# Kernel tuning notes

Hardware: AMD Instinct MI355X
Metric: run time of the kernel (lower is better)

## Reference

```python
import jax, jax.numpy as jnp
import numpy as np

B, T, U = 8, 200, 50
EPROJS = 512
DUNITS = 512
EMB = 512
JOINT = 512
ODIM = 1000
BLANK = 0


def setup_inputs() -> dict:
    key = jax.random.key(0)
    ks = jax.random.split(key, 16)
    s = lambda k, shape: (jax.random.normal(k, shape, jnp.float32) * 0.05)
    inp = {
        "hs_pad": jax.random.normal(ks[0], (B, T, EPROJS), jnp.float32),
        "ys_in_pad": jax.random.randint(ks[1], (B, U), 0, ODIM),
        "emb": s(ks[2], (ODIM, EMB)),
        "W_ih_0": s(ks[3], (4 * DUNITS, EMB)),
        "W_hh_0": s(ks[4], (4 * DUNITS, DUNITS)),
        "b_ih_0": s(ks[5], (4 * DUNITS,)),
        "b_hh_0": s(ks[6], (4 * DUNITS,)),
        "W_ih_1": s(ks[7], (4 * DUNITS, DUNITS)),
        "W_hh_1": s(ks[8], (4 * DUNITS, DUNITS)),
        "b_ih_1": s(ks[9], (4 * DUNITS,)),
        "b_hh_1": s(ks[10], (4 * DUNITS,)),
        "W_enc": s(ks[11], (JOINT, EPROJS)),
        "b_enc": s(ks[12], (JOINT,)),
        "W_dec": s(ks[13], (JOINT, DUNITS)),
        "W_out": s(ks[14], (ODIM, JOINT)),
        "b_out": s(ks[15], (ODIM,)),
    }
    return inp


def _lstm_cell(x, h, c, W_ih, W_hh, b_ih, b_hh):
    # torch.nn.LSTMCell, gate order i, f, g, o
    gates = x @ W_ih.T + b_ih + h @ W_hh.T + b_hh
    i, f, g, o = jnp.split(gates, 4, axis=-1)
    c_new = jax.nn.sigmoid(f) * c + jax.nn.sigmoid(i) * jnp.tanh(g)
    h_new = jax.nn.sigmoid(o) * jnp.tanh(c_new)
    return h_new, c_new


def reference(hs_pad, ys_in_pad, emb, W_ih_0, W_hh_0, b_ih_0, b_hh_0,
              W_ih_1, W_hh_1, b_ih_1, b_hh_1, W_enc, b_enc, W_dec,
              W_out, b_out):
    # embedding with padding_idx=blank -> blank row is zero
    emb_tbl = emb.at[BLANK].set(0.0)
    eys = emb_tbl[ys_in_pad]            # (B, U, EMB)

    def step(carry, ey):
        h0, c0, h1, c1 = carry
        h0, c0 = _lstm_cell(ey, h0, c0, W_ih_0, W_hh_0, b_ih_0, b_hh_0)
        h1, c1 = _lstm_cell(h0, h1, c1, W_ih_1, W_hh_1, b_ih_1, b_hh_1)
        return (h0, c0, h1, c1), h1

    z0 = jnp.zeros((hs_pad.shape[0], DUNITS), hs_pad.dtype)
    _, h_dec = jax.lax.scan(step, (z0, z0, z0, z0),
                            jnp.swapaxes(eys, 0, 1))   # (U, B, D)
    h_dec = jnp.swapaxes(h_dec, 0, 1)                  # (B, U, D)

    # joint: project first, then broadcast-add (avoids (B,T,U,Henc) expand)
    z_enc = hs_pad @ W_enc.T + b_enc                   # (B, T, J)
    z_dec = h_dec @ W_dec.T                            # (B, U, J), no bias
    z = jnp.tanh(z_enc[:, :, None, :] + z_dec[:, None, :, :])  # (B,T,U,J)
    return z @ W_out.T + b_out                         # (B, T, U, ODIM)
```

## Files before the change

kernel.cpp:

```cpp
#include <hip/hip_runtime.h>
#include <cstdint>
#include <cstddef>

#define Tsz 200
#define Usz 50
#define Kd  512
#define G4h 2048
#define OD  1000

typedef __attribute__((ext_vector_type(8))) short short8;
typedef __attribute__((ext_vector_type(4))) short s16x4;
typedef __attribute__((ext_vector_type(4))) float f32x4;

__device__ __forceinline__ unsigned short f2bf(float x) {
  union { float f; unsigned u; } v; v.f = x;
  unsigned r = v.u + 0x7FFFu + ((v.u >> 16) & 1u);
  return (unsigned short)(r >> 16);
}
__device__ __forceinline__ float bf2f(unsigned short h) {
  union { unsigned u; float f; } v; v.u = ((unsigned)h) << 16; return v.f;
}
__device__ __forceinline__ void splits(float w, short& hi, short& lo) {
  unsigned short h = f2bf(w);
  hi = (short)h;
  lo = (short)f2bf(w - bf2f(h));
}
__device__ __forceinline__ void split8(float4 f0, float4 f1, short8& hi, short8& lo) {
  float v[8] = {f0.x, f0.y, f0.z, f0.w, f1.x, f1.y, f1.z, f1.w};
  #pragma unroll
  for (int i = 0; i < 8; ++i) { short a, b2; splits(v[i], a, b2); hi[i] = a; lo[i] = b2; }
}
__device__ __forceinline__ float ftanh(float x) {
  float ax = fabsf(x);
  float t = __expf(-2.0f * ax);
  float r = (1.0f - t) / (1.0f + t);
  return copysignf(r, x);
}
__device__ __forceinline__ float sigf(float x) {
  return 1.0f / (1.0f + __expf(-x));
}
__device__ __forceinline__ void astore(unsigned* p, unsigned v) {
  __hip_atomic_store(p, v, __ATOMIC_RELAXED, __HIP_MEMORY_SCOPE_AGENT);
}
__device__ __forceinline__ void gload16(const void* g, void* l) {
  __builtin_amdgcn_global_load_lds(
      (const __attribute__((address_space(1))) void*)g,
      (__attribute__((address_space(3))) void*)l, 16, 0, 0);
}
__device__ __forceinline__ void aload4x4(const unsigned* p0, const unsigned* p1,
                                         const unsigned* p2, const unsigned* p3,
                                         uint4& r0, uint4& r1, uint4& r2, uint4& r3) {
  asm volatile(
      "global_load_dwordx4 %0, %4, off sc0 sc1\n\t"
      "global_load_dwordx4 %1, %5, off sc0 sc1\n\t"
      "global_load_dwordx4 %2, %6, off sc0 sc1\n\t"
      "global_load_dwordx4 %3, %7, off sc0 sc1\n\t"
      "s_waitcnt vmcnt(0)"
      : "=&v"(r0), "=&v"(r1), "=&v"(r2), "=&v"(r3)
      : "v"(p0), "v"(p1), "v"(p2), "v"(p3)
      : "memory");
}
__device__ __forceinline__ void aload8x4(const unsigned* p0, const unsigned* p1,
                                         const unsigned* p2, const unsigned* p3,
                                         const unsigned* q0, const unsigned* q1,
                                         const unsigned* q2, const unsigned* q3,
                                         uint4& r0, uint4& r1, uint4& r2, uint4& r3,
                                         uint4& s0, uint4& s1, uint4& s2, uint4& s3) {
  asm volatile(
      "global_load_dwordx4 %0, %8, off sc0 sc1\n\t"
      "global_load_dwordx4 %1, %9, off sc0 sc1\n\t"
      "global_load_dwordx4 %2, %10, off sc0 sc1\n\t"
      "global_load_dwordx4 %3, %11, off sc0 sc1\n\t"
      "global_load_dwordx4 %4, %12, off sc0 sc1\n\t"
      "global_load_dwordx4 %5, %13, off sc0 sc1\n\t"
      "global_load_dwordx4 %6, %14, off sc0 sc1\n\t"
      "global_load_dwordx4 %7, %15, off sc0 sc1\n\t"
      "s_waitcnt vmcnt(0)"
      : "=&v"(r0), "=&v"(r1), "=&v"(r2), "=&v"(r3),
        "=&v"(s0), "=&v"(s1), "=&v"(s2), "=&v"(s3)
      : "v"(p0), "v"(p1), "v"(p2), "v"(p3),
        "v"(q0), "v"(q1), "v"(q2), "v"(q3)
      : "memory");
}
__device__ __forceinline__ unsigned tagbad4(uint4 v, unsigned tg) {
  return ((v.x ^ tg) | (v.y ^ tg) | (v.z ^ tg) | (v.w ^ tg)) & 0xFFu;
}

__global__ __launch_bounds__(256) void k_prep(
    const int* __restrict__ ys, const float* __restrict__ emb,
    const float* __restrict__ Wih0, const float* __restrict__ bih0,
    const float* __restrict__ bhh0, const float* __restrict__ hs,
    const float* __restrict__ Wenc, const float* __restrict__ benc,
    const float* __restrict__ Wout,
    unsigned* __restrict__ h0s, unsigned* __restrict__ h1s,
    unsigned short* __restrict__ Wb, float* __restrict__ zenc,
    float* __restrict__ xgr) {
  __shared__ float Al[16 * 516];
  __shared__ int idxs[16];
  const int bid = blockIdx.x;
  const int tid = threadIdx.x;

  if (bid < 16) {
    int i = bid * 256 + tid;
    if (i < 4096) { h0s[i] = 0u; h1s[i] = 0u; }
    return;
  }
  if (bid < 272) {
    int idx = (bid - 16) * 256 + tid;
    int n = idx >> 6, chunk = idx & 63;
    short8 v;
    if (n < OD) {
      const float* src = Wout + (size_t)n * Kd + chunk * 8;
      #pragma unroll
      for (int j = 0; j < 8; ++j) v[j] = (short)f2bf(src[j]);
    } else {
      #pragma unroll
      for (int j = 0; j < 8; ++j) v[j] = 0;
    }
    int tile = n >> 5, srow = n & 31;
    size_t off = (size_t)tile * 32768 + srow * 1024 +
                 ((chunk * 16) ^ ((srow & 7) << 4));
    *(short8*)((char*)Wb + off) = v;
    return;
  }
  if (bid < 1072) {
    int q = bid - 272;
    int m0 = (q % 100) * 16;
    int n0 = (q / 100) * 64;
    for (int i = tid; i < 16 * 512; i += 256) {
      int r = i >> 9, k = i & 511;
      Al[r * 516 + k] = hs[(size_t)(m0 + r) * Kd + k];
    }
    __syncthreads();
    int nl = tid & 63;
    int mg = (tid >> 6) * 4;
    int n = n0 + nl;
    const float* Wr = Wenc + (size_t)n * Kd;
    float acc[4] = {0.f, 0.f, 0.f, 0.f};
    #pragma unroll 4
    for (int k = 0; k < 512; k += 4) {
      float4 w = *(const float4*)(Wr + k);
      #pragma unroll
      for (int j = 0; j < 4; ++j) {
        const float* ar = &Al[(mg + j) * 516 + k];
        acc[j] += ar[0] * w.x + ar[1] * w.y + ar[2] * w.z + ar[3] * w.w;
      }
    }
    float bias = benc[n];
    #pragma unroll
    for (int j = 0; j < 4; ++j)
      zenc[(size_t)(m0 + mg + j) * 512 + n] = acc[j] + bias;
    return;
  }
  {
    int q = bid - 1072;
    int m0 = (q % 25) * 16;
    int n0 = (q / 25) * 64;
    if (tid < 16) {
      int m = m0 + tid;
      int u = m >> 3, b = m & 7;
      idxs[tid] = ys[b * Usz + u];
    }
    __syncthreads();
    for (int i = tid; i < 16 * 512; i += 256) {
      int r = i >> 9, k = i & 511;
      int idx = idxs[r];
      Al[r * 516 + k] = (idx == 0) ? 0.0f : emb[(size_t)idx * Kd + k];
    }
    __syncthreads();
    int nl = tid & 63;
    int mg = (tid >> 6) * 4;
    int n = n0 + nl;
    const float* Wr = Wih0 + (size_t)n * Kd;
    float acc[4] = {0.f, 0.f, 0.f, 0.f};
    #pragma unroll 4
    for (int k = 0; k < 512; k += 4) {
      float4 w = *(const float4*)(Wr + k);
      #pragma unroll
      for (int j = 0; j < 4; ++j) {
        const float* ar = &Al[(mg + j) * 516 + k];
        acc[j] += ar[0] * w.x + ar[1] * w.y + ar[2] * w.z + ar[3] * w.w;
      }
    }
    float bias = bih0[n] + bhh0[n];
    int g = n >> 9, jc = n & 511;
    #pragma unroll
    for (int j = 0; j < 4; ++j) {
      int m = m0 + mg + j;
      int u = m >> 3, b = m & 7;
      xgr[(((size_t)u * 32 + (jc >> 4)) * 4 + g) * 128 + (jc & 15) * 8 + b] =
          acc[j] + bias;
    }
  }
}

__global__ __launch_bounds__(256) void k_gemm(const float* __restrict__ A,
                                              const float* __restrict__ W,
                                              float* __restrict__ C, int N) {
  __shared__ float Al[16 * 516];
  int m0 = blockIdx.x * 16;
  int n0 = blockIdx.y * 64;
  for (int i = threadIdx.x; i < 16 * 512; i += 256) {
    int r = i >> 9, k = i & 511;
    Al[r * 516 + k] = A[(size_t)(m0 + r) * Kd + k];
  }
  __syncthreads();
  int nl = threadIdx.x & 63;
  int mg = (threadIdx.x >> 6) * 4;
  int n = n0 + nl;
  const float* Wr = W + (size_t)n * Kd;
  float acc[4] = {0.f, 0.f, 0.f, 0.f};
  #pragma unroll 4
  for (int k = 0; k < 512; k += 4) {
    float4 w = *(const float4*)(Wr + k);
    #pragma unroll
    for (int j = 0; j < 4; ++j) {
      const float* ar = &Al[(mg + j) * 516 + k];
      acc[j] += ar[0] * w.x + ar[1] * w.y + ar[2] * w.z + ar[3] * w.w;
    }
  }
  #pragma unroll
  for (int j = 0; j < 4; ++j)
    C[(size_t)(m0 + mg + j) * N + n] = acc[j];
}

__global__ __launch_bounds__(256, 1) void k_lstm_all(
    const float* __restrict__ Whh0, const float* __restrict__ Wih1,
    const float* __restrict__ Whh1, const float* __restrict__ bih1,
    const float* __restrict__ bhh1, const float* __restrict__ xgr,
    unsigned* __restrict__ h0s, unsigned* __restrict__ h1s,
    float* __restrict__ hdec) {
  __shared__ __align__(16) unsigned short sd[34816];
  unsigned short* H0H = sd;
  unsigned short* H0L = sd + 8192;
  unsigned short* H1H = sd + 16384;
  unsigned short* H1L = sd + 24576;
  float* gsm = (float*)(sd + 32768);

  const int tid = threadIdx.x;
  const int lane = tid & 63;
  const int wv = tid >> 6;
  const int bid = blockIdx.x;
  const int kq = lane >> 4;
  const int cl = lane & 15;
  const int gg = (tid & 127) >> 1;
  const int sub = (tid & 1) << 3;
  const int swz = (gg & 7) << 4;
  const int gbase = gg << 8;
  const int tb = tid >> 7;

  if (bid < 32) {
    const int j0 = bid * 16;
    short8 whi[16], wlo[16];
    {
      const float* wr = Whh0 + ((size_t)(wv * 512 + j0 + cl)) * Kd;
      #pragma unroll
      for (int kt = 0; kt < 16; ++kt) {
        const float* p4 = wr + kt * 32 + kq * 8;
        split8(*(const float4*)p4, *(const float4*)(p4 + 4), whi[kt], wlo[kt]);
      }
    }
    float creg = 0.0f;
    const int ejl = tid & 15, eb = (tid >> 4) & 7;
    for (int p = 0; p < 50; ++p) {
      const float* xp = xgr + (((size_t)p * 32 + bid) * 4) * 128 + ejl * 8 + eb;
      float x0 = xp[0], x1 = xp[128], x2 = xp[256], x3 = xp[384];
      {
        const unsigned* bp = h0s + (size_t)p * 4096 + (tid << 2);
        uint4 v0, v1, v2, v3;
        aload4x4(bp, bp + 1024, bp + 2048, bp + 3072, v0, v1, v2, v3);
        const unsigned tg = (unsigned)p;
        for (int guard = 0; guard < (1 << 18); ++guard) {
          unsigned bad = tagbad4(v0, tg) | tagbad4(v1, tg) |
                         tagbad4(v2, tg) | tagbad4(v3, tg);
          if (!bad) break;
          __builtin_amdgcn_s_sleep(1);
          aload4x4(bp, bp + 1024, bp + 2048, bp + 3072, v0, v1, v2, v3);
        }
        unsigned uu[4][4] = {{v0.x, v0.y, v0.z, v0.w}, {v1.x, v1.y, v1.z, v1.w},
                             {v2.x, v2.y, v2.z, v2.w}, {v3.x, v3.y, v3.z, v3.w}};
        #pragma unroll
        for (int j = 0; j < 4; ++j) {
          s16x4 hv, lv;
          #pragma unroll
          for (int e = 0; e < 4; ++e) {
            short hh, ll; splits(__uint_as_float(uu[j][e]), hh, ll);
            hv[e] = hh; lv[e] = ll;
          }
          int b = j * 2 + tb;
          int off = gbase + (((b << 4) + sub) ^ swz);
          *(s16x4*)((char*)H0H + off) = hv;
          *(s16x4*)((char*)H0L + off) = lv;
        }
      }
      __syncthreads();
      f32x4 accA = {0.f, 0.f, 0.f, 0.f};
      f32x4 accB = {0.f, 0.f, 0.f, 0.f};
      f32x4 accC = {0.f, 0.f, 0.f, 0.f};
      #pragma unroll
      for (int kt = 0; kt < 16; ++kt) {
        int g = kt * 4 + kq;
        int off = (g << 8) + ((cl << 4) ^ ((g & 7) << 4));
        short8 bh = *(const short8*)((const char*)H0H + off);
        short8 bl = *(const short8*)((const char*)H0L + off);
        accA = __builtin_amdgcn_mfma_f32_16x16x32_bf16(whi[kt], bh, accA, 0, 0, 0);
        accB = __builtin_amdgcn_mfma_f32_16x16x32_bf16(wlo[kt], bh, accB, 0, 0, 0);
        accC = __builtin_amdgcn_mfma_f32_16x16x32_bf16(whi[kt], bl, accC, 0, 0, 0);
      }
      f32x4 acc = (accA + accB) + accC;
      *(f32x4*)&gsm[(wv * 16 + cl) * 16 + kq * 4] = acc;
      __syncthreads();
      if (tid < 128) {
        float g0 = gsm[(0 * 16 + eb) * 16 + ejl];
        float g1 = gsm[(1 * 16 + eb) * 16 + ejl];
        float g2 = gsm[(2 * 16 + eb) * 16 + ejl];
        float g3 = gsm[(3 * 16 + eb) * 16 + ejl];
        float gi = g0 + x0;
        float gf = g1 + x1;
        float gg2 = g2 + x2;
        float go = g3 + x3;
        float cn = sigf(gf) * creg + sigf(gi) * ftanh(gg2);
        float hn = sigf(go) * ftanh(cn);
        creg = cn;
        unsigned hv = (__float_as_uint(hn) & ~0xFFu) | (unsigned)(p + 1);
        astore(h0s + (size_t)(p + 1) * 4096 + eb * 512 + j0 + ejl, hv);
      }
      __syncthreads();
    }
  } else {
    const int j0 = (bid - 32) * 8;
    const int mt = wv & 1, kh = wv >> 1;
    short8 wihh[8], wihl[8], whhh[8], whhl[8];
    {
      const int g = mt * 2 + (cl >> 3), jl = cl & 7;
      const float* wr0 = Wih1 + ((size_t)(g * 512 + j0 + jl)) * Kd;
      const float* wr1 = Whh1 + ((size_t)(g * 512 + j0 + jl)) * Kd;
      #pragma unroll
      for (int k2 = 0; k2 < 8; ++k2) {
        int kt = kh * 8 + k2;
        const float* p0 = wr0 + kt * 32 + kq * 8;
        const float* p1 = wr1 + kt * 32 + kq * 8;
        split8(*(const float4*)p0, *(const float4*)(p0 + 4), wihh[k2], wihl[k2]);
        split8(*(const float4*)p1, *(const float4*)(p1 + 4), whhh[k2], whhl[k2]);
      }
    }
    float creg = 0.0f;
    const int ejl = tid & 7, eb = (tid >> 3) & 7;
    float bs0 = bih1[0 * 512 + j0 + ejl] + bhh1[0 * 512 + j0 + ejl];
    float bs1 = bih1[1 * 512 + j0 + ejl] + bhh1[1 * 512 + j0 + ejl];
    float bs2 = bih1[2 * 512 + j0 + ejl] + bhh1[2 * 512 + j0 + ejl];
    float bs3 = bih1[3 * 512 + j0 + ejl] + bhh1[3 * 512 + j0 + ejl];
    for (int p = 1; p <= 50; ++p) {
      {
        const unsigned* bp0 = h0s + (size_t)p * 4096 + (tid << 2);
        const unsigned* bp1 = h1s + (size_t)(p - 1) * 4096 + (tid << 2);
        uint4 v0, v1, v2, v3, w0, w1, w2, w3;
        aload8x4(bp0, bp0 + 1024, bp0 + 2048, bp0 + 3072,
                 bp1, bp1 + 1024, bp1 + 2048, bp1 + 3072,
                 v0, v1, v2, v3, w0, w1, w2, w3);
        const unsigned tg0 = (unsigned)p, tg1 = (unsigned)(p - 1);
        for (int guard = 0; guard < (1 << 18); ++guard) {
          unsigned bad = tagbad4(v0, tg0) | tagbad4(v1, tg0) |
                         tagbad4(v2, tg0) | tagbad4(v3, tg0) |
                         tagbad4(w0, tg1) | tagbad4(w1, tg1) |
                         tagbad4(w2, tg1) | tagbad4(w3, tg1);
          if (!bad) break;
          __builtin_amdgcn_s_sleep(1);
          aload8x4(bp0, bp0 + 1024, bp0 + 2048, bp0 + 3072,
                   bp1, bp1 + 1024, bp1 + 2048, bp1 + 3072,
                   v0, v1, v2, v3, w0, w1, w2, w3);
        }
        unsigned uu[4][4] = {{v0.x, v0.y, v0.z, v0.w}, {v1.x, v1.y, v1.z, v1.w},
                             {v2.x, v2.y, v2.z, v2.w}, {v3.x, v3.y, v3.z, v3.w}};
        unsigned tt[4][4] = {{w0.x, w0.y, w0.z, w0.w}, {w1.x, w1.y, w1.z, w1.w},
                             {w2.x, w2.y, w2.z, w2.w}, {w3.x, w3.y, w3.z, w3.w}};
        #pragma unroll
        for (int j = 0; j < 4; ++j) {
          s16x4 hv, lv, hw, lw;
          #pragma unroll
          for (int e = 0; e < 4; ++e) {
            short hh, ll;
            splits(__uint_as_float(uu[j][e]), hh, ll); hv[e] = hh; lv[e] = ll;
            splits(__uint_as_float(tt[j][e]), hh, ll); hw[e] = hh; lw[e] = ll;
          }
          int b = j * 2 + tb;
          int off = gbase + (((b << 4) + sub) ^ swz);
          *(s16x4*)((char*)H0H + off) = hv;
          *(s16x4*)((char*)H0L + off) = lv;
          *(s16x4*)((char*)H1H + off) = hw;
          *(s16x4*)((char*)H1L + off) = lw;
        }
      }
      __syncthreads();
      f32x4 q0 = {0.f,0.f,0.f,0.f}, q1 = {0.f,0.f,0.f,0.f}, q2 = {0.f,0.f,0.f,0.f};
      f32x4 q3 = {0.f,0.f,0.f,0.f}, q4 = {0.f,0.f,0.f,0.f}, q5 = {0.f,0.f,0.f,0.f};
      #pragma unroll
      for (int k2 = 0; k2 < 8; ++k2) {
        int kt = kh * 8 + k2;
        int g = kt * 4 + kq;
        int off = (g << 8) + ((cl << 4) ^ ((g & 7) << 4));
        short8 b0h = *(const short8*)((const char*)H0H + off);
        short8 b0l = *(const short8*)((const char*)H0L + off);
        short8 b1h = *(const short8*)((const char*)H1H + off);
        short8 b1l = *(const short8*)((const char*)H1L + off);
        q0 = __builtin_amdgcn_mfma_f32_16x16x32_bf16(wihh[k2], b0h, q0, 0, 0, 0);
        q1 = __builtin_amdgcn_mfma_f32_16x16x32_bf16(wihl[k2], b0h, q1, 0, 0, 0);
        q2 = __builtin_amdgcn_mfma_f32_16x16x32_bf16(wihh[k2], b0l, q2, 0, 0, 0);
        q3 = __builtin_amdgcn_mfma_f32_16x16x32_bf16(whhh[k2], b1h, q3, 0, 0, 0);
        q4 = __builtin_amdgcn_mfma_f32_16x16x32_bf16(whhl[k2], b1h, q4, 0, 0, 0);
        q5 = __builtin_amdgcn_mfma_f32_16x16x32_bf16(whhh[k2], b1l, q5, 0, 0, 0);
      }
      f32x4 acc = ((q0 + q1) + (q2 + q3)) + (q4 + q5);
      *(f32x4*)&gsm[(wv * 16 + cl) * 16 + kq * 4] = acc;
      __syncthreads();
      if (tid < 64) {
        float gv[4];
        #pragma unroll
        for (int g = 0; g < 4; ++g) {
          int mtg = g >> 1, r = (g & 1) * 8 + ejl;
          gv[g] = gsm[(mtg * 16 + eb) * 16 + r] + gsm[((2 + mtg) * 16 + eb) * 16 + r];
        }
        float gi = gv[0] + bs0, gf = gv[1] + bs1, gg2 = gv[2] + bs2, go = gv[3] + bs3;
        float cn = sigf(gf) * creg + sigf(gi) * ftanh(gg2);
        float hn = sigf(go) * ftanh(cn);
        creg = cn;
        int jg = j0 + ejl;
        unsigned hv = (__float_as_uint(hn) & ~0xFFu) | (unsigned)p;
        astore(h1s + (size_t)p * 4096 + eb * 512 + jg, hv);
        hdec[((size_t)eb * Usz + (p - 1)) * Kd + jg] = __uint_as_float(hv);
      }
      __syncthreads();
    }
  }
}

__global__ __launch_bounds__(256) void k_joint(const float* __restrict__ zenc,
                                               const float* __restrict__ zdec,
                                               const unsigned short* __restrict__ Wb,
                                               const float* __restrict__ bout,
                                               float* __restrict__ out) {
  __shared__ __align__(16) unsigned short Blds[2 * 16384];
  const int lane = threadIdx.x & 63;
  const int wv = threadIdx.x >> 6;
  const int kgrp = lane >> 4;
  const int rl = lane & 15;
  const int rbase = blockIdx.x * 64 + wv * 16;

  short8 a[16];
  {
    int row = rbase + rl;
    int u = row % Usz;
    int bt = row / Usz;
    const float* ze = zenc + (size_t)bt * Kd;
    const float* zd = zdec + (size_t)((bt / Tsz) * Usz + u) * Kd;
    #pragma unroll
    for (int kk = 0; kk < 16; ++kk) {
      int k0 = kk * 32 + kgrp * 8;
      float4 e0 = *(const float4*)(ze + k0);
      float4 e1 = *(const float4*)(ze + k0 + 4);
      float4 d0 = *(const float4*)(zd + k0);
      float4 d1 = *(const float4*)(zd + k0 + 4);
      short8 tt;
      tt[0] = (short)f2bf(ftanh(e0.x + d0.x));
      tt[1] = (short)f2bf(ftanh(e0.y + d0.y));
      tt[2] = (short)f2bf(ftanh(e0.z + d0.z));
      tt[3] = (short)f2bf(ftanh(e0.w + d0.w));
      tt[4] = (short)f2bf(ftanh(e1.x + d1.x));
      tt[5] = (short)f2bf(ftanh(e1.y + d1.y));
      tt[6] = (short)f2bf(ftanh(e1.z + d1.z));
      tt[7] = (short)f2bf(ftanh(e1.w + d1.w));
      a[kk] = tt;
    }
  }

  #pragma unroll
  for (int i = 0; i < 8; ++i) {
    int o = (i * 4 + wv) * 1024;
    gload16((const char*)Wb + o + lane * 16, (char*)Blds + o);
  }
  asm volatile("s_waitcnt vmcnt(0)" ::: "memory");
  __builtin_amdgcn_s_barrier();
  __builtin_amdgcn_sched_barrier(0);

  int cur = 0;
  for (int it = 0; it < 32; ++it) {
    if (it < 31) {
      const char* g = (const char*)Wb + (size_t)(it + 1) * 32768;
      char* l = (char*)Blds + (cur ^ 1) * 32768;
      #pragma unroll
      for (int i = 0; i < 8; ++i) {
        int o = (i * 4 + wv) * 1024;
        gload16(g + o + lane * 16, l + o);
      }
      __builtin_amdgcn_sched_barrier(0);
    }
    const char* bufc = (const char*)Blds + cur * 32768;
    int n0 = it * 32;
    f32x4 acc0 = {0.f, 0.f, 0.f, 0.f};
    f32x4 acc1 = {0.f, 0.f, 0.f, 0.f};
    #pragma unroll
    for (int kk = 0; kk < 16; ++kk) {
      int c = kk * 4 + kgrp;
      int b0 = ((c * 16) ^ ((rl & 7) << 4)) + rl * 1024;
      int b1 = ((c * 16) ^ ((rl & 7) << 4)) + (rl + 16) * 1024;
      short8 bf0 = *(const short8*)(bufc + b0);
      short8 bf1 = *(const short8*)(bufc + b1);
      acc0 = __builtin_amdgcn_mfma_f32_16x16x32_bf16(a[kk], bf0, acc0, 0, 0, 0);
      acc1 = __builtin_amdgcn_mfma_f32_16x16x32_bf16(a[kk], bf1, acc1, 0, 0, 0);
    }
    #pragma unroll
    for (int nt = 0; nt < 2; ++nt) {
      int n = n0 + nt * 16 + rl;
      if (n < OD) {
        float bo = bout[n];
        const f32x4& A0 = nt ? acc1 : acc0;
        size_t r0 = (size_t)(rbase + kgrp * 4) * OD + n;
        #pragma unroll
        for (int j = 0; j < 4; ++j)
          out[r0 + (size_t)j * OD] = A0[j] + bo;
      }
    }
    if (it < 31) {
      __builtin_amdgcn_sched_barrier(0);
      asm volatile("s_waitcnt vmcnt(8)" ::: "memory");
      __builtin_amdgcn_s_barrier();
      __builtin_amdgcn_sched_barrier(0);
    }
    cur ^= 1;
  }
}

extern "C" void kernel_launch(void* const* d_in, const int* in_sizes, int n_in,
                              void* d_out, int out_size, void* d_ws, size_t ws_size,
                              hipStream_t stream) {
  const float* hs   = (const float*)d_in[0];
  const int*   ys   = (const int*)d_in[1];
  const float* emb  = (const float*)d_in[2];
  const float* Wih0 = (const float*)d_in[3];
  const float* Whh0 = (const float*)d_in[4];
  const float* bih0 = (const float*)d_in[5];
  const float* bhh0 = (const float*)d_in[6];
  const float* Wih1 = (const float*)d_in[7];
  const float* Whh1 = (const float*)d_in[8];
  const float* bih1 = (const float*)d_in[9];
  const float* bhh1 = (const float*)d_in[10];
  const float* Wenc = (const float*)d_in[11];
  const float* benc = (const float*)d_in[12];
  const float* Wdec = (const float*)d_in[13];
  const float* Wout = (const float*)d_in[14];
  const float* bout = (const float*)d_in[15];
  float* out = (float*)d_out;

  float* ws   = (float*)d_ws;
  float* xgr  = ws + 204800;
  float* zenc = ws + 1024000;
  float* zdec = ws + 1843200;
  float* hdec = ws + 2048000;
  unsigned short* Wb = (unsigned short*)(ws + 2252800);
  unsigned* h0s = (unsigned*)(ws + 2514944);
  unsigned* h1s = (unsigned*)(ws + 2723840);

  k_prep<<<1872, 256, 0, stream>>>(ys, emb, Wih0, bih0, bhh0, hs, Wenc, benc,
                                   Wout, h0s, h1s, Wb, zenc, xgr);
  k_lstm_all<<<96, 256, 0, stream>>>(Whh0, Wih1, Whh1, bih1, bhh1, xgr,
                                     h0s, h1s, hdec);
  k_gemm<<<dim3(25, 8), 256, 0, stream>>>(hdec, Wdec, zdec, 512);
  k_joint<<<1250, 256, 0, stream>>>(zenc, zdec, Wb, bout, out);
}
```

Measured before the change: 406.8 us.

## Overlap encoder projection with LSTM kernel and use 32x32 MFMA in joint

```diff
diff --git a/kernel.cpp b/kernel.cpp
--- a/kernel.cpp
+++ b/kernel.cpp
@@ -11,6 +11,7 @@
 typedef __attribute__((ext_vector_type(8))) short short8;
 typedef __attribute__((ext_vector_type(4))) short s16x4;
 typedef __attribute__((ext_vector_type(4))) float f32x4;
+typedef __attribute__((ext_vector_type(16))) float f32x16;
 
 __device__ __forceinline__ unsigned short f2bf(float x) {
   union { float f; unsigned u; } v; v.f = x;
@@ -89,11 +90,8 @@
 __global__ __launch_bounds__(256) void k_prep(
     const int* __restrict__ ys, const float* __restrict__ emb,
     const float* __restrict__ Wih0, const float* __restrict__ bih0,
-    const float* __restrict__ bhh0, const float* __restrict__ hs,
-    const float* __restrict__ Wenc, const float* __restrict__ benc,
-    const float* __restrict__ Wout,
+    const float* __restrict__ bhh0,
     unsigned* __restrict__ h0s, unsigned* __restrict__ h1s,
-    unsigned short* __restrict__ Wb, float* __restrict__ zenc,
     float* __restrict__ xgr) {
   __shared__ float Al[16 * 516];
   __shared__ int idxs[16];
@@ -105,92 +103,43 @@
     if (i < 4096) { h0s[i] = 0u; h1s[i] = 0u; }
     return;
   }
-  if (bid < 272) {
-    int idx = (bid - 16) * 256 + tid;
-    int n = idx >> 6, chunk = idx & 63;
-    short8 v;
-    if (n < OD) {
-      const float* src = Wout + (size_t)n * Kd + chunk * 8;
-      #pragma unroll
-      for (int j = 0; j < 8; ++j) v[j] = (short)f2bf(src[j]);
-    } else {
-      #pragma unroll
-      for (int j = 0; j < 8; ++j) v[j] = 0;
-    }
-    int tile = n >> 5, srow = n & 31;
-    size_t off = (size_t)tile * 32768 + srow * 1024 +
-                 ((chunk * 16) ^ ((srow & 7) << 4));
-    *(short8*)((char*)Wb + off) = v;
-    return;
-  }
-  if (bid < 1072) {
-    int q = bid - 272;
-    int m0 = (q % 100) * 16;
-    int n0 = (q / 100) * 64;
-    for (int i = tid; i < 16 * 512; i += 256) {
-      int r = i >> 9, k = i & 511;
-      Al[r * 516 + k] = hs[(size_t)(m0 + r) * Kd + k];
-    }
-    __syncthreads();
-    int nl = tid & 63;
-    int mg = (tid >> 6) * 4;
-    int n = n0 + nl;
-    const float* Wr = Wenc + (size_t)n * Kd;
-    float acc[4] = {0.f, 0.f, 0.f, 0.f};
-    #pragma unroll 4
-    for (int k = 0; k < 512; k += 4) {
-      float4 w = *(const float4*)(Wr + k);
-      #pragma unroll
-      for (int j = 0; j < 4; ++j) {
-        const float* ar = &Al[(mg + j) * 516 + k];
-        acc[j] += ar[0] * w.x + ar[1] * w.y + ar[2] * w.z + ar[3] * w.w;
-      }
-    }
-    float bias = benc[n];
-    #pragma unroll
-    for (int j = 0; j < 4; ++j)
-      zenc[(size_t)(m0 + mg + j) * 512 + n] = acc[j] + bias;
-    return;
-  }
-  {
-    int q = bid - 1072;
-    int m0 = (q % 25) * 16;
-    int n0 = (q / 25) * 64;
-    if (tid < 16) {
-      int m = m0 + tid;
-      int u = m >> 3, b = m & 7;
-      idxs[tid] = ys[b * Usz + u];
-    }
-    __syncthreads();
-    for (int i = tid; i < 16 * 512; i += 256) {
-      int r = i >> 9, k = i & 511;
-      int idx = idxs[r];
-      Al[r * 516 + k] = (idx == 0) ? 0.0f : emb[(size_t)idx * Kd + k];
-    }
-    __syncthreads();
-    int nl = tid & 63;
-    int mg = (tid >> 6) * 4;
-    int n = n0 + nl;
-    const float* Wr = Wih0 + (size_t)n * Kd;
-    float acc[4] = {0.f, 0.f, 0.f, 0.f};
-    #pragma unroll 4
-    for (int k = 0; k < 512; k += 4) {
-      float4 w = *(const float4*)(Wr + k);
-      #pragma unroll
-      for (int j = 0; j < 4; ++j) {
-        const float* ar = &Al[(mg + j) * 516 + k];
-        acc[j] += ar[0] * w.x + ar[1] * w.y + ar[2] * w.z + ar[3] * w.w;
-      }
-    }
-    float bias = bih0[n] + bhh0[n];
-    int g = n >> 9, jc = n & 511;
+  int q = bid - 16;
+  int m0 = (q % 25) * 16;
+  int n0 = (q / 25) * 64;
+  if (tid < 16) {
+    int m = m0 + tid;
+    int u = m >> 3, b = m & 7;
+    idxs[tid] = ys[b * Usz + u];
+  }
+  __syncthreads();
+  for (int i = tid; i < 16 * 512; i += 256) {
+    int r = i >> 9, k = i & 511;
+    int idx = idxs[r];
+    Al[r * 516 + k] = (idx == 0) ? 0.0f : emb[(size_t)idx * Kd + k];
+  }
+  __syncthreads();
+  int nl = tid & 63;
+  int mg = (tid >> 6) * 4;
+  int n = n0 + nl;
+  const float* Wr = Wih0 + (size_t)n * Kd;
+  float acc[4] = {0.f, 0.f, 0.f, 0.f};
+  #pragma unroll 4
+  for (int k = 0; k < 512; k += 4) {
+    float4 w = *(const float4*)(Wr + k);
     #pragma unroll
     for (int j = 0; j < 4; ++j) {
-      int m = m0 + mg + j;
-      int u = m >> 3, b = m & 7;
-      xgr[(((size_t)u * 32 + (jc >> 4)) * 4 + g) * 128 + (jc & 15) * 8 + b] =
-          acc[j] + bias;
-    }
+      const float* ar = &Al[(mg + j) * 516 + k];
+      acc[j] += ar[0] * w.x + ar[1] * w.y + ar[2] * w.z + ar[3] * w.w;
+    }
+  }
+  float bias = bih0[n] + bhh0[n];
+  int g = n >> 9, jc = n & 511;
+  #pragma unroll
+  for (int j = 0; j < 4; ++j) {
+    int m = m0 + mg + j;
+    int u = m >> 3, b = m & 7;
+    xgr[(((size_t)u * 32 + (jc >> 4)) * 4 + g) * 128 + (jc & 15) * 8 + b] =
+        acc[j] + bias;
   }
 }
 
@@ -224,12 +173,15 @@
     C[(size_t)(m0 + mg + j) * N + n] = acc[j];
 }
 
-__global__ __launch_bounds__(256, 1) void k_lstm_all(
+__global__ __launch_bounds__(256, 1) void k_lstm_zenc(
     const float* __restrict__ Whh0, const float* __restrict__ Wih1,
     const float* __restrict__ Whh1, const float* __restrict__ bih1,
     const float* __restrict__ bhh1, const float* __restrict__ xgr,
     unsigned* __restrict__ h0s, unsigned* __restrict__ h1s,
-    float* __restrict__ hdec) {
+    float* __restrict__ hdec,
+    const float* __restrict__ Wout, unsigned short* __restrict__ Wb,
+    const float* __restrict__ hs, const float* __restrict__ Wenc,
+    const float* __restrict__ benc, float* __restrict__ zenc) {
   __shared__ __align__(16) unsigned short sd[34816];
   unsigned short* H0H = sd;
   unsigned short* H0L = sd + 8192;
@@ -241,6 +193,56 @@
   const int lane = tid & 63;
   const int wv = tid >> 6;
   const int bid = blockIdx.x;
+
+  if (bid >= 352) {
+    float* Al = (float*)sd;
+    int q = bid - 352;
+    int m0 = (q % 100) * 16;
+    int n0 = (q / 100) * 64;
+    for (int i = tid; i < 16 * 512; i += 256) {
+      int r = i >> 9, k = i & 511;
+      Al[r * 516 + k] = hs[(size_t)(m0 + r) * Kd + k];
+    }
+    __syncthreads();
+    int nl = tid & 63;
+    int mg = (tid >> 6) * 4;
+    int n = n0 + nl;
+    const float* Wr = Wenc + (size_t)n * Kd;
+    float acc[4] = {0.f, 0.f, 0.f, 0.f};
+    #pragma unroll 4
+    for (int k = 0; k < 512; k += 4) {
+      float4 w = *(const float4*)(Wr + k);
+      #pragma unroll
+      for (int j = 0; j < 4; ++j) {
+        const float* ar = &Al[(mg + j) * 516 + k];
+        acc[j] += ar[0] * w.x + ar[1] * w.y + ar[2] * w.z + ar[3] * w.w;
+      }
+    }
+    float bias = benc[n];
+    #pragma unroll
+    for (int j = 0; j < 4; ++j)
+      zenc[(size_t)(m0 + mg + j) * 512 + n] = acc[j] + bias;
+    return;
+  }
+  if (bid >= 96) {
+    int idx = (bid - 96) * 256 + tid;
+    int n = idx >> 6, chunk = idx & 63;
+    short8 v;
+    if (n < OD) {
+      const float* src = Wout + (size_t)n * Kd + chunk * 8;
+      #pragma unroll
+      for (int j = 0; j < 8; ++j) v[j] = (short)f2bf(src[j]);
+    } else {
+      #pragma unroll
+      for (int j = 0; j < 8; ++j) v[j] = 0;
+    }
+    int tile = n >> 5, srow = n & 31;
+    size_t off = (size_t)tile * 32768 + srow * 1024 +
+                 ((chunk * 16) ^ (srow << 4));
+    *(short8*)((char*)Wb + off) = v;
+    return;
+  }
+
   const int kq = lane >> 4;
   const int cl = lane & 15;
   const int gg = (tid & 127) >> 1;
@@ -434,28 +436,31 @@
   }
 }
 
-__global__ __launch_bounds__(256) void k_joint(const float* __restrict__ zenc,
-                                               const float* __restrict__ zdec,
-                                               const unsigned short* __restrict__ Wb,
-                                               const float* __restrict__ bout,
-                                               float* __restrict__ out) {
+__global__ __launch_bounds__(256, 1) void k_joint(
+    const float* __restrict__ zenc, const float* __restrict__ zdec,
+    const unsigned short* __restrict__ Wb, const float* __restrict__ bout,
+    float* __restrict__ out) {
   __shared__ __align__(16) unsigned short Blds[2 * 16384];
+  __shared__ float blds[1024];
   const int lane = threadIdx.x & 63;
   const int wv = threadIdx.x >> 6;
-  const int kgrp = lane >> 4;
-  const int rl = lane & 15;
-  const int rbase = blockIdx.x * 64 + wv * 16;
-
-  short8 a[16];
+  const int r32 = lane & 31;
+  const int kh = lane >> 5;
+  const int rbase = blockIdx.x * 128 + wv * 32;
+
+  for (int i = threadIdx.x; i < 1024; i += 256)
+    blds[i] = (i < OD) ? bout[i] : 0.0f;
+
+  short8 a[32];
   {
-    int row = rbase + rl;
+    int row = rbase + r32;
     int u = row % Usz;
     int bt = row / Usz;
     const float* ze = zenc + (size_t)bt * Kd;
     const float* zd = zdec + (size_t)((bt / Tsz) * Usz + u) * Kd;
     #pragma unroll
-    for (int kk = 0; kk < 16; ++kk) {
-      int k0 = kk * 32 + kgrp * 8;
+    for (int kt = 0; kt < 32; ++kt) {
+      int k0 = kt * 16 + kh * 8;
       float4 e0 = *(const float4*)(ze + k0);
       float4 e1 = *(const float4*)(ze + k0 + 4);
       float4 d0 = *(const float4*)(zd + k0);
@@ -469,7 +474,7 @@
       tt[5] = (short)f2bf(ftanh(e1.y + d1.y));
       tt[6] = (short)f2bf(ftanh(e1.z + d1.z));
       tt[7] = (short)f2bf(ftanh(e1.w + d1.w));
-      a[kk] = tt;
+      a[kt] = tt;
     }
   }
 
@@ -496,33 +501,33 @@
     }
     const char* bufc = (const char*)Blds + cur * 32768;
     int n0 = it * 32;
-    f32x4 acc0 = {0.f, 0.f, 0.f, 0.f};
-    f32x4 acc1 = {0.f, 0.f, 0.f, 0.f};
+    f32x16 accE = {0.f,0.f,0.f,0.f,0.f,0.f,0.f,0.f,0.f,0.f,0.f,0.f,0.f,0.f,0.f,0.f};
+    f32x16 accO = {0.f,0.f,0.f,0.f,0.f,0.f,0.f,0.f,0.f,0.f,0.f,0.f,0.f,0.f,0.f,0.f};
     #pragma unroll
-    for (int kk = 0; kk < 16; ++kk) {
-      int c = kk * 4 + kgrp;
-      int b0 = ((c * 16) ^ ((rl & 7) << 4)) + rl * 1024;
-      int b1 = ((c * 16) ^ ((rl & 7) << 4)) + (rl + 16) * 1024;
-      short8 bf0 = *(const short8*)(bufc + b0);
-      short8 bf1 = *(const short8*)(bufc + b1);
-      acc0 = __builtin_amdgcn_mfma_f32_16x16x32_bf16(a[kk], bf0, acc0, 0, 0, 0);
-      acc1 = __builtin_amdgcn_mfma_f32_16x16x32_bf16(a[kk], bf1, acc1, 0, 0, 0);
-    }
-    #pragma unroll
-    for (int nt = 0; nt < 2; ++nt) {
-      int n = n0 + nt * 16 + rl;
-      if (n < OD) {
-        float bo = bout[n];
-        const f32x4& A0 = nt ? acc1 : acc0;
-        size_t r0 = (size_t)(rbase + kgrp * 4) * OD + n;
-        #pragma unroll
-        for (int j = 0; j < 4; ++j)
-          out[r0 + (size_t)j * OD] = A0[j] + bo;
+    for (int kt = 0; kt < 32; kt += 2) {
+      int c0 = kt * 2 + kh;
+      int c1 = c0 + 2;
+      int o0 = r32 * 1024 + ((c0 * 16) ^ (r32 << 4));
+      int o1 = r32 * 1024 + ((c1 * 16) ^ (r32 << 4));
+      short8 b0 = *(const short8*)(bufc + o0);
+      short8 b1 = *(const short8*)(bufc + o1);
+      accE = __builtin_amdgcn_mfma_f32_32x32x16_bf16(a[kt], b0, accE, 0, 0, 0);
+      accO = __builtin_amdgcn_mfma_f32_32x32x16_bf16(a[kt + 1], b1, accO, 0, 0, 0);
+    }
+    f32x16 acc = accE + accO;
+    int n = n0 + r32;
+    float bo = blds[n];
+    if (n < OD) {
+      size_t base = (size_t)(rbase + kh * 4) * OD + n;
+      #pragma unroll
+      for (int reg = 0; reg < 16; ++reg) {
+        int r = (reg & 3) + 8 * (reg >> 2);
+        out[base + (size_t)r * OD] = acc[reg] + bo;
       }
     }
     if (it < 31) {
       __builtin_amdgcn_sched_barrier(0);
-      asm volatile("s_waitcnt vmcnt(8)" ::: "memory");
+      asm volatile("s_waitcnt vmcnt(16)" ::: "memory");
       __builtin_amdgcn_s_barrier();
       __builtin_amdgcn_sched_barrier(0);
     }
@@ -560,10 +565,10 @@
   unsigned* h0s = (unsigned*)(ws + 2514944);
   unsigned* h1s = (unsigned*)(ws + 2723840);
 
-  k_prep<<<1872, 256, 0, stream>>>(ys, emb, Wih0, bih0, bhh0, hs, Wenc, benc,
-                                   Wout, h0s, h1s, Wb, zenc, xgr);
-  k_lstm_all<<<96, 256, 0, stream>>>(Whh0, Wih1, Whh1, bih1, bhh1, xgr,
-                                     h0s, h1s, hdec);
+  k_prep<<<816, 256, 0, stream>>>(ys, emb, Wih0, bih0, bhh0, h0s, h1s, xgr);
+  k_lstm_zenc<<<1152, 256, 0, stream>>>(Whh0, Wih1, Whh1, bih1, bhh1, xgr,
+                                        h0s, h1s, hdec, Wout, Wb,
+                                        hs, Wenc, benc, zenc);
   k_gemm<<<dim3(25, 8), 256, 0, stream>>>(hdec, Wdec, zdec, 512);
-  k_joint<<<1250, 256, 0, stream>>>(zenc, zdec, Wb, bout, out);
-}
+  k_joint<<<625, 256, 0, stream>>>(zenc, zdec, Wb, bout, out);
+}
```

New measurement: 437.9 us. 1.08x slower.

## Fuse LSTM, decoder projection and joint into one kernel with per-step flag handoff

Applied to the files above, without the earlier changes.

```diff
diff --git a/kernel.cpp b/kernel.cpp
--- a/kernel.cpp
+++ b/kernel.cpp
@@ -46,6 +46,12 @@
   __builtin_amdgcn_global_load_lds(
       (const __attribute__((address_space(1))) void*)g,
       (__attribute__((address_space(3))) void*)l, 16, 0, 0);
+}
+__device__ __forceinline__ uint4 aload1(const unsigned* p) {
+  uint4 r;
+  asm volatile("global_load_dwordx4 %0, %1, off sc0 sc1\n\ts_waitcnt vmcnt(0)"
+               : "=&v"(r) : "v"(p) : "memory");
+  return r;
 }
 __device__ __forceinline__ void aload4x4(const unsigned* p0, const unsigned* p1,
                                          const unsigned* p2, const unsigned* p3,
@@ -194,53 +200,184 @@
   }
 }
 
-__global__ __launch_bounds__(256) void k_gemm(const float* __restrict__ A,
-                                              const float* __restrict__ W,
-                                              float* __restrict__ C, int N) {
-  __shared__ float Al[16 * 516];
-  int m0 = blockIdx.x * 16;
-  int n0 = blockIdx.y * 64;
-  for (int i = threadIdx.x; i < 16 * 512; i += 256) {
-    int r = i >> 9, k = i & 511;
-    Al[r * 516 + k] = A[(size_t)(m0 + r) * Kd + k];
-  }
-  __syncthreads();
-  int nl = threadIdx.x & 63;
-  int mg = (threadIdx.x >> 6) * 4;
-  int n = n0 + nl;
-  const float* Wr = W + (size_t)n * Kd;
-  float acc[4] = {0.f, 0.f, 0.f, 0.f};
-  #pragma unroll 4
-  for (int k = 0; k < 512; k += 4) {
-    float4 w = *(const float4*)(Wr + k);
-    #pragma unroll
-    for (int j = 0; j < 4; ++j) {
-      const float* ar = &Al[(mg + j) * 516 + k];
-      acc[j] += ar[0] * w.x + ar[1] * w.y + ar[2] * w.z + ar[3] * w.w;
-    }
-  }
-  #pragma unroll
-  for (int j = 0; j < 4; ++j)
-    C[(size_t)(m0 + mg + j) * N + n] = acc[j];
-}
-
-__global__ __launch_bounds__(256, 1) void k_lstm_all(
+__global__ __launch_bounds__(256, 1) void k_mega(
     const float* __restrict__ Whh0, const float* __restrict__ Wih1,
     const float* __restrict__ Whh1, const float* __restrict__ bih1,
     const float* __restrict__ bhh1, const float* __restrict__ xgr,
     unsigned* __restrict__ h0s, unsigned* __restrict__ h1s,
-    float* __restrict__ hdec) {
-  __shared__ __align__(16) unsigned short sd[34816];
-  unsigned short* H0H = sd;
-  unsigned short* H0L = sd + 8192;
-  unsigned short* H1H = sd + 16384;
-  unsigned short* H1L = sd + 24576;
-  float* gsm = (float*)(sd + 32768);
+    const float* __restrict__ Wdec, unsigned* __restrict__ zdu,
+    const float* __restrict__ zenc, const unsigned short* __restrict__ Wb,
+    const float* __restrict__ bout, float* __restrict__ out) {
+  __shared__ __align__(16) unsigned char smem[69632];
 
   const int tid = threadIdx.x;
   const int lane = tid & 63;
   const int wv = tid >> 6;
   const int bid = blockIdx.x;
+
+  if (bid >= 146) {
+    unsigned short* Blds = (unsigned short*)smem;
+    float* zdl = (float*)(smem + 65536);
+    const int q = bid - 146;
+    const int u = q / 25;
+    const int g = q % 25;
+    const int kgrp = lane >> 4;
+    const int rl = lane & 15;
+    const int btbase = g * 64 + wv * 16;
+
+    #pragma unroll
+    for (int i = 0; i < 8; ++i) {
+      int o = (i * 4 + wv) * 1024;
+      gload16((const char*)Wb + o + lane * 16, (char*)smem + o);
+    }
+
+    const int b_lo = (g * 64) / 200;
+    const int b_hi = (g * 64 + 63) / 200;
+    {
+      int rsel = tid >> 7;
+      int bb = rsel ? b_hi : b_lo;
+      const unsigned* zp = zdu + ((size_t)(bb * 50 + u) << 9) + ((tid & 127) << 2);
+      const unsigned tg = (unsigned)(u + 1) & 0xFFu;
+      uint4 v = aload1(zp);
+      for (int guard = 0; guard < (1 << 20); ++guard) {
+        if (tagbad4(v, tg) == 0) break;
+        __builtin_amdgcn_s_sleep(4);
+        v = aload1(zp);
+      }
+      *(uint4*)&zdl[rsel * 512 + (tid & 127) * 4] = v;
+    }
+    __syncthreads();
+
+    short8 a[16];
+    {
+      int bt = btbase + rl;
+      int sel = ((bt / 200) != b_lo) ? 1 : 0;
+      const float* ze = zenc + (size_t)bt * Kd;
+      const float* zd = &zdl[sel * 512];
+      #pragma unroll
+      for (int kk = 0; kk < 16; ++kk) {
+        int k0 = kk * 32 + kgrp * 8;
+        float4 e0 = *(const float4*)(ze + k0);
+        float4 e1 = *(const float4*)(ze + k0 + 4);
+        float4 d0 = *(const float4*)(zd + k0);
+        float4 d1 = *(const float4*)(zd + k0 + 4);
+        short8 tt;
+        tt[0] = (short)f2bf(ftanh(e0.x + d0.x));
+        tt[1] = (short)f2bf(ftanh(e0.y + d0.y));
+        tt[2] = (short)f2bf(ftanh(e0.z + d0.z));
+        tt[3] = (short)f2bf(ftanh(e0.w + d0.w));
+        tt[4] = (short)f2bf(ftanh(e1.x + d1.x));
+        tt[5] = (short)f2bf(ftanh(e1.y + d1.y));
+        tt[6] = (short)f2bf(ftanh(e1.z + d1.z));
+        tt[7] = (short)f2bf(ftanh(e1.w + d1.w));
+        a[kk] = tt;
+      }
+    }
+    asm volatile("s_waitcnt vmcnt(0) lgkmcnt(0)" ::: "memory");
+    __builtin_amdgcn_s_barrier();
+    __builtin_amdgcn_sched_barrier(0);
+
+    int cur = 0;
+    for (int it = 0; it < 32; ++it) {
+      if (it < 31) {
+        const char* gptr = (const char*)Wb + (size_t)(it + 1) * 32768;
+        char* l = (char*)smem + (cur ^ 1) * 32768;
+        #pragma unroll
+        for (int i = 0; i < 8; ++i) {
+          int o = (i * 4 + wv) * 1024;
+          gload16(gptr + o + lane * 16, l + o);
+        }
+        __builtin_amdgcn_sched_barrier(0);
+      }
+      const char* bufc = (const char*)smem + cur * 32768;
+      int n0 = it * 32;
+      f32x4 acc0 = {0.f, 0.f, 0.f, 0.f};
+      f32x4 acc1 = {0.f, 0.f, 0.f, 0.f};
+      #pragma unroll
+      for (int kk = 0; kk < 16; ++kk) {
+        int c = kk * 4 + kgrp;
+        int o0 = ((c * 16) ^ ((rl & 7) << 4)) + rl * 1024;
+        int o1 = ((c * 16) ^ ((rl & 7) << 4)) + (rl + 16) * 1024;
+        short8 bf0 = *(const short8*)(bufc + o0);
+        short8 bf1 = *(const short8*)(bufc + o1);
+        acc0 = __builtin_amdgcn_mfma_f32_16x16x32_bf16(a[kk], bf0, acc0, 0, 0, 0);
+        acc1 = __builtin_amdgcn_mfma_f32_16x16x32_bf16(a[kk], bf1, acc1, 0, 0, 0);
+      }
+      #pragma unroll
+      for (int nt = 0; nt < 2; ++nt) {
+        int n = n0 + nt * 16 + rl;
+        if (n < OD) {
+          float bo = bout[n];
+          const f32x4& A0 = nt ? acc1 : acc0;
+          size_t r0 = ((size_t)(btbase + kgrp * 4) * 50 + u) * OD + n;
+          #pragma unroll
+          for (int j = 0; j < 4; ++j)
+            out[r0 + (size_t)j * 50 * OD] = A0[j] + bo;
+        }
+      }
+      if (it < 31) {
+        __builtin_amdgcn_sched_barrier(0);
+        asm volatile("s_waitcnt vmcnt(8)" ::: "memory");
+        __builtin_amdgcn_s_barrier();
+        __builtin_amdgcn_sched_barrier(0);
+      }
+      cur ^= 1;
+    }
+    return;
+  }
+  if (bid >= 96) {
+    float* hl = (float*)smem;
+    const int u = bid - 96;
+    const int p = u + 1;
+    {
+      const unsigned* bp = h1s + (size_t)p * 4096 + tid * 16;
+      uint4 v0, v1, v2, v3;
+      aload4x4(bp, bp + 4, bp + 8, bp + 12, v0, v1, v2, v3);
+      const unsigned tg = (unsigned)p & 0xFFu;
+      for (int guard = 0; guard < (1 << 20); ++guard) {
+        unsigned bad = tagbad4(v0, tg) | tagbad4(v1, tg) |
+                       tagbad4(v2, tg) | tagbad4(v3, tg);
+        if (!bad) break;
+        __builtin_amdgcn_s_sleep(4);
+        aload4x4(bp, bp + 4, bp + 8, bp + 12, v0, v1, v2, v3);
+      }
+      *(uint4*)&hl[tid * 16] = v0;
+      *(uint4*)&hl[tid * 16 + 4] = v1;
+      *(uint4*)&hl[tid * 16 + 8] = v2;
+      *(uint4*)&hl[tid * 16 + 12] = v3;
+    }
+    __syncthreads();
+    const int n2 = tid * 2;
+    const float* w0p = Wdec + (size_t)n2 * Kd;
+    const float* w1p = w0p + Kd;
+    float acc0[8] = {0,0,0,0,0,0,0,0};
+    float acc1[8] = {0,0,0,0,0,0,0,0};
+    #pragma unroll 4
+    for (int kc = 0; kc < 128; ++kc) {
+      float4 w0 = *(const float4*)(w0p + kc * 4);
+      float4 w1 = *(const float4*)(w1p + kc * 4);
+      #pragma unroll
+      for (int b = 0; b < 8; ++b) {
+        float4 h4 = *(const float4*)&hl[b * 512 + kc * 4];
+        acc0[b] += w0.x * h4.x + w0.y * h4.y + w0.z * h4.z + w0.w * h4.w;
+        acc1[b] += w1.x * h4.x + w1.y * h4.y + w1.z * h4.z + w1.w * h4.w;
+      }
+    }
+    const unsigned tg = (unsigned)p;
+    #pragma unroll
+    for (int b = 0; b < 8; ++b) {
+      size_t base = ((size_t)(b * 50 + u) << 9);
+      astore(zdu + base + n2, (__float_as_uint(acc0[b]) & ~0xFFu) | tg);
+      astore(zdu + base + n2 + 1, (__float_as_uint(acc1[b]) & ~0xFFu) | tg);
+    }
+    return;
+  }
+
+  unsigned short* H0H = (unsigned short*)smem;
+  unsigned short* H0L = H0H + 8192;
+  unsigned short* H1H = H0H + 16384;
+  unsigned short* H1L = H0H + 24576;
+  float* gsm = (float*)(H0H + 32768);
   const int kq = lane >> 4;
   const int cl = lane & 15;
   const int gg = (tid & 127) >> 1;
@@ -427,106 +564,9 @@
         int jg = j0 + ejl;
         unsigned hv = (__float_as_uint(hn) & ~0xFFu) | (unsigned)p;
         astore(h1s + (size_t)p * 4096 + eb * 512 + jg, hv);
-        hdec[((size_t)eb * Usz + (p - 1)) * Kd + jg] = __uint_as_float(hv);
       }
       __syncthreads();
     }
-  }
-}
-
-__global__ __launch_bounds__(256) void k_joint(const float* __restrict__ zenc,
-                                               const float* __restrict__ zdec,
-                                               const unsigned short* __restrict__ Wb,
-                                               const float* __restrict__ bout,
-                                               float* __restrict__ out) {
-  __shared__ __align__(16) unsigned short Blds[2 * 16384];
-  const int lane = threadIdx.x & 63;
-  const int wv = threadIdx.x >> 6;
-  const int kgrp = lane >> 4;
-  const int rl = lane & 15;
-  const int rbase = blockIdx.x * 64 + wv * 16;
-
-  short8 a[16];
-  {
-    int row = rbase + rl;
-    int u = row % Usz;
-    int bt = row / Usz;
-    const float* ze = zenc + (size_t)bt * Kd;
-    const float* zd = zdec + (size_t)((bt / Tsz) * Usz + u) * Kd;
-    #pragma unroll
-    for (int kk = 0; kk < 16; ++kk) {
-      int k0 = kk * 32 + kgrp * 8;
-      float4 e0 = *(const float4*)(ze + k0);
-      float4 e1 = *(const float4*)(ze + k0 + 4);
-      float4 d0 = *(const float4*)(zd + k0);
-      float4 d1 = *(const float4*)(zd + k0 + 4);
-      short8 tt;
-      tt[0] = (short)f2bf(ftanh(e0.x + d0.x));
-      tt[1] = (short)f2bf(ftanh(e0.y + d0.y));
-      tt[2] = (short)f2bf(ftanh(e0.z + d0.z));
-      tt[3] = (short)f2bf(ftanh(e0.w + d0.w));
-      tt[4] = (short)f2bf(ftanh(e1.x + d1.x));
-      tt[5] = (short)f2bf(ftanh(e1.y + d1.y));
-      tt[6] = (short)f2bf(ftanh(e1.z + d1.z));
-      tt[7] = (short)f2bf(ftanh(e1.w + d1.w));
-      a[kk] = tt;
-    }
-  }
-
-  #pragma unroll
-  for (int i = 0; i < 8; ++i) {
-    int o = (i * 4 + wv) * 1024;
-    gload16((const char*)Wb + o + lane * 16, (char*)Blds + o);
-  }
-  asm volatile("s_waitcnt vmcnt(0)" ::: "memory");
-  __builtin_amdgcn_s_barrier();
-  __builtin_amdgcn_sched_barrier(0);
-
-  int cur = 0;
-  for (int it = 0; it < 32; ++it) {
-    if (it < 31) {
-      const char* g = (const char*)Wb + (size_t)(it + 1) * 32768;
-      char* l = (char*)Blds + (cur ^ 1) * 32768;
-      #pragma unroll
-      for (int i = 0; i < 8; ++i) {
-        int o = (i * 4 + wv) * 1024;
-        gload16(g + o + lane * 16, l + o);
-      }
-      __builtin_amdgcn_sched_barrier(0);
-    }
-    const char* bufc = (const char*)Blds + cur * 32768;
-    int n0 = it * 32;
-    f32x4 acc0 = {0.f, 0.f, 0.f, 0.f};
-    f32x4 acc1 = {0.f, 0.f, 0.f, 0.f};
-    #pragma unroll
-    for (int kk = 0; kk < 16; ++kk) {
-      int c = kk * 4 + kgrp;
-      int b0 = ((c * 16) ^ ((rl & 7) << 4)) + rl * 1024;
-      int b1 = ((c * 16) ^ ((rl & 7) << 4)) + (rl + 16) * 1024;
-      short8 bf0 = *(const short8*)(bufc + b0);
-      short8 bf1 = *(const short8*)(bufc + b1);
-      acc0 = __builtin_amdgcn_mfma_f32_16x16x32_bf16(a[kk], bf0, acc0, 0, 0, 0);
-      acc1 = __builtin_amdgcn_mfma_f32_16x16x32_bf16(a[kk], bf1, acc1, 0, 0, 0);
-    }
-    #pragma unroll
-    for (int nt = 0; nt < 2; ++nt) {
-      int n = n0 + nt * 16 + rl;
-      if (n < OD) {
-        float bo = bout[n];
-        const f32x4& A0 = nt ? acc1 : acc0;
-        size_t r0 = (size_t)(rbase + kgrp * 4) * OD + n;
-        #pragma unroll
-        for (int j = 0; j < 4; ++j)
-          out[r0 + (size_t)j * OD] = A0[j] + bo;
-      }
-    }
-    if (it < 31) {
-      __builtin_amdgcn_sched_barrier(0);
-      asm volatile("s_waitcnt vmcnt(8)" ::: "memory");
-      __builtin_amdgcn_s_barrier();
-      __builtin_amdgcn_sched_barrier(0);
-    }
-    cur ^= 1;
   }
 }
 
@@ -554,16 +594,13 @@
   float* ws   = (float*)d_ws;
   float* xgr  = ws + 204800;
   float* zenc = ws + 1024000;
-  float* zdec = ws + 1843200;
-  float* hdec = ws + 2048000;
+  unsigned* zdu = (unsigned*)(ws + 1843200);
   unsigned short* Wb = (unsigned short*)(ws + 2252800);
   unsigned* h0s = (unsigned*)(ws + 2514944);
   unsigned* h1s = (unsigned*)(ws + 2723840);
 
   k_prep<<<1872, 256, 0, stream>>>(ys, emb, Wih0, bih0, bhh0, hs, Wenc, benc,
                                    Wout, h0s, h1s, Wb, zenc, xgr);
-  k_lstm_all<<<96, 256, 0, stream>>>(Whh0, Wih1, Whh1, bih1, bhh1, xgr,
-                                     h0s, h1s, hdec);
-  k_gemm<<<dim3(25, 8), 256, 0, stream>>>(hdec, Wdec, zdec, 512);
-  k_joint<<<1250, 256, 0, stream>>>(zenc, zdec, Wb, bout, out);
-}
+  k_mega<<<1396, 256, 0, stream>>>(Whh0, Wih1, Whh1, bih1, bhh1, xgr,
+                                   h0s, h1s, Wdec, zdu, zenc, Wb, bout, out);
+}
```

New measurement: 384.7 us. 1.06x faster.
